# Performance work log

Measured on AMD Instinct MI355X. Metric: run time of the kernel, lower is better.

Reference implementation:

```python
import jax, jax.numpy as jnp
import numpy as np

N = 50000
E = 1600000
HID = 128
H = 8
D = HID // H


def _layer_norm(x, g, b, eps=1e-5):
    mu = jnp.mean(x, axis=-1, keepdims=True)
    var = jnp.mean(jnp.square(x - mu), axis=-1, keepdims=True)
    return (x - mu) * jax.lax.rsqrt(var + eps) * g + b


def setup_inputs() -> dict:
    key = jax.random.key(0)
    ks = jax.random.split(key, 20)
    s = 1.0 / np.sqrt(HID)
    inp = {
        "x": jax.random.normal(ks[0], (N, HID), jnp.float32),
        "edge_index": jax.random.randint(ks[1], (2, E), 0, N, jnp.int64),
        "edge_attr": jax.random.randint(ks[2], (E,), 0, 13, jnp.int64),
        # projections (stored as [in, out] so y = x @ W + b)
        "Wq": jax.random.normal(ks[3], (HID, HID), jnp.float32) * s,
        "bq": jnp.zeros((HID,), jnp.float32),
        "Wk": jax.random.normal(ks[4], (HID, HID), jnp.float32) * s,
        "bk": jnp.zeros((HID,), jnp.float32),
        "Wv": jax.random.normal(ks[5], (HID, HID), jnp.float32) * s,
        "bv": jnp.zeros((HID,), jnp.float32),
        "Wo": jax.random.normal(ks[6], (HID, HID), jnp.float32) * s,
        "bo": jnp.zeros((HID,), jnp.float32),
        "edge_bias_table": jax.random.normal(ks[7], (13, H), jnp.float32) * 0.02,
        "W1": jax.random.normal(ks[8], (HID, 4 * HID), jnp.float32) * s,
        "b1": jnp.zeros((4 * HID,), jnp.float32),
        "W2": jax.random.normal(ks[9], (4 * HID, HID), jnp.float32) * (0.5 * s),
        "b2": jnp.zeros((HID,), jnp.float32),
        "g1": jnp.ones((HID,), jnp.float32),
        "be1": jnp.zeros((HID,), jnp.float32),
        "g2": jnp.ones((HID,), jnp.float32),
        "be2": jnp.zeros((HID,), jnp.float32),
    }
    return inp


def reference(x, edge_index, edge_attr, Wq, bq, Wk, bk, Wv, bv, Wo, bo,
              edge_bias_table, W1, b1, W2, b2, g1, be1, g2, be2):
    n = x.shape[0]
    residual = x
    h = _layer_norm(x, g1, be1)
    Q = (h @ Wq + bq).reshape(n, H, D)
    K = (h @ Wk + bk).reshape(n, H, D)
    V = (h @ Wv + bv).reshape(n, H, D)
    src, dst = edge_index[0], edge_index[1]
    # per-edge scores [E, H]
    scores = jnp.sum(Q[dst] * K[src], axis=-1) / np.sqrt(D)
    scores = scores + edge_bias_table[jnp.clip(edge_attr, 0, 12)]
    # scatter softmax over incoming edges of each dst (global max, as in source)
    scores_exp = jnp.exp(scores - jnp.max(scores))
    attn_sum = jax.ops.segment_sum(scores_exp, dst, num_segments=n)  # [N, H]
    attn_w = scores_exp / (attn_sum[dst] + 1e-8)                      # [E, H]
    messages = V[src] * attn_w[..., None]                             # [E, H, D]
    out = jax.ops.segment_sum(messages, dst, num_segments=n)          # [N, H, D]
    out = out.reshape(n, HID) @ Wo + bo
    x = residual + out  # dropout is identity in eval
    residual = x
    h2 = _layer_norm(x, g2, be2)
    ffn = jax.nn.relu(h2 @ W1 + b1) @ W2 + b2
    return residual + ffn
```

## Files before the change

### kernel.cpp

```cpp
#include <hip/hip_runtime.h>
#include <hip/hip_bf16.h>

#define N_NODES 50000
#define E_EDGES 1600000
#define HID 128
#define NH 8
#define HD 16

#define NBKT 196
#define BKT_CAP 9216
#define CHUNK_A 4096
#define EPT 16
#define BINA_BLOCKS ((E_EDGES + CHUNK_A - 1) / CHUNK_A)
#define WCVT_BLOCKS 771
#define LN_BLOCKS 12500

using short8 = __attribute__((ext_vector_type(8))) short;
using f32x4  = __attribute__((ext_vector_type(4))) float;
using f32x2  = __attribute__((ext_vector_type(2))) float;
typedef _Float16 h16x2 __attribute__((ext_vector_type(2)));

#if defined(__has_builtin) && __has_builtin(__builtin_amdgcn_fdot2)
#define FDOT2(a, b, c) __builtin_amdgcn_fdot2((a), (b), (c), false)
#else
__device__ __forceinline__ float FDOT2(h16x2 a, h16x2 b, float c) {
    return fmaf((float)a[0], (float)b[0], fmaf((float)a[1], (float)b[1], c));
}
#endif

__device__ __forceinline__ float wave_reduce_sum(float v) {
    #pragma unroll
    for (int off = 32; off > 0; off >>= 1) v += __shfl_xor(v, off, 64);
    return v;
}

__device__ __forceinline__ unsigned int packbf2(float a, float b) {
    __hip_bfloat162 t;
    t.x = __float2bfloat16(a);
    t.y = __float2bfloat16(b);
    unsigned int u;
    __builtin_memcpy(&u, &t, 4);
    return u;
}

__device__ __forceinline__ unsigned char fp8e(float v) {
    return (unsigned char)(__builtin_amdgcn_cvt_pk_fp8_f32(v, v, 0u, false) & 0xFFu);
}

union U4H {
    uint4 u;
    h16x2 h[4];
};

struct KV {
    U4H k0, k1;
    uint4 v;
};

__global__ __launch_bounds__(256) void prep_kernel(
    const int* __restrict__ ei, const int* __restrict__ attr,
    int* __restrict__ bcur, unsigned int* __restrict__ temp,
    const float* __restrict__ Wq, const float* __restrict__ Wk,
    const float* __restrict__ Wv, const float* __restrict__ Wo,
    const float* __restrict__ W1, const float* __restrict__ W2,
    const float* __restrict__ bq, const float* __restrict__ bk,
    const float* __restrict__ bv,
    __hip_bfloat16* __restrict__ Wqkvt, __hip_bfloat16* __restrict__ Wot,
    __hip_bfloat16* __restrict__ W1t, __hip_bfloat16* __restrict__ W2t,
    float* __restrict__ bqkv,
    const float* __restrict__ x, const float* __restrict__ g1,
    const float* __restrict__ be1, __hip_bfloat16* __restrict__ h_out) {
    __shared__ unsigned int sval[CHUNK_A];
    __shared__ unsigned short sbkt[CHUNK_A];
    __shared__ int hist[NBKT];
    __shared__ int lofs[NBKT];
    __shared__ int gbase[NBKT];
    __shared__ int lcur[NBKT];
    __shared__ int sc[256];
    const int b = blockIdx.x;
    const int tid = threadIdx.x;
    if (b < BINA_BLOCKS) {
        const int e0 = b * CHUNK_A;
        const int n = min(CHUNK_A, E_EDGES - e0);
        for (int i = tid; i < NBKT; i += 256) hist[i] = 0;
        __syncthreads();
        unsigned int v[EPT];
        short bk_[EPT];
        #pragma unroll
        for (int j = 0; j < EPT; ++j) {
            int i = tid + j * 256;
            bk_[j] = -1;
            v[j] = 0;
            if (i < n) {
                int e = e0 + i;
                int src = ei[e];
                int dst = ei[E_EDGES + e];
                int a = attr[e]; a = min(max(a, 0), 12);
                v[j] = (unsigned)src | ((unsigned)a << 16) | ((unsigned)(dst & 255) << 20);
                int bb = dst >> 8;
                bk_[j] = (short)bb;
                atomicAdd(&hist[bb], 1);
            }
        }
        __syncthreads();
        sc[tid] = (tid < NBKT) ? hist[tid] : 0;
        __syncthreads();
        for (int off = 1; off < 256; off <<= 1) {
            int xx = (tid >= off) ? sc[tid - off] : 0;
            __syncthreads();
            sc[tid] += xx;
            __syncthreads();
        }
        if (tid < NBKT) {
            int h = hist[tid];
            lofs[tid] = sc[tid] - h;
            lcur[tid] = 0;
            gbase[tid] = h ? atomicAdd(&bcur[tid], h) : 0;
        }
        __syncthreads();
        #pragma unroll
        for (int j = 0; j < EPT; ++j) {
            if (bk_[j] >= 0) {
                int p = lofs[bk_[j]] + atomicAdd(&lcur[bk_[j]], 1);
                sval[p] = v[j];
                sbkt[p] = (unsigned short)bk_[j];
            }
        }
        __syncthreads();
        for (int i = tid; i < n; i += 256) {
            int bb = sbkt[i];
            temp[(size_t)bb * BKT_CAP + gbase[bb] + (i - lofs[bb])] = sval[i];
        }
    } else if (b < BINA_BLOCKS + WCVT_BLOCKS) {
        int t = (b - BINA_BLOCKS) * 256 + tid;
        if (t >= 196608) {
            int i = t - 196608;
            if (i < 384) bqkv[i] = i < 128 ? bq[i] : (i < 256 ? bk[i - 128] : bv[i - 256]);
            return;
        }
        const float* W; __hip_bfloat16* Wt; int K, N, idx;
        if (t < 65536) {
            int which = t >> 14; idx = t & 16383; K = 128; N = 128;
            W = which == 0 ? Wq : which == 1 ? Wk : which == 2 ? Wv : Wo;
            Wt = which == 3 ? Wot : Wqkvt + which * 16384;
        } else if (t < 131072) { idx = t - 65536;  K = 128; N = 512; W = W1; Wt = W1t; }
        else                   { idx = t - 131072; K = 512; N = 128; W = W2; Wt = W2t; }
        int n = idx / K, k = idx - n * K;
        Wt[idx] = __float2bfloat16(W[(size_t)k * N + n]);
    } else {
        int wave = tid >> 6;
        int lane = tid & 63;
        int row = (b - BINA_BLOCKS - WCVT_BLOCKS) * 4 + wave;
        if (row >= N_NODES) return;
        float2 v = ((const float2*)(x + (size_t)row * HID))[lane];
        float s = wave_reduce_sum(v.x + v.y);
        float mu = s * (1.0f / HID);
        float dx = v.x - mu, dy = v.y - mu;
        float q = wave_reduce_sum(dx * dx + dy * dy);
        float rstd = rsqrtf(q * (1.0f / HID) + 1e-5f);
        float2 gg = ((const float2*)g1)[lane];
        float2 bb = ((const float2*)be1)[lane];
        __hip_bfloat162 o;
        o.x = __float2bfloat16(dx * rstd * gg.x + bb.x);
        o.y = __float2bfloat16(dy * rstd * gg.y + bb.y);
        ((__hip_bfloat162*)(h_out + (size_t)row * HID))[lane] = o;
    }
}

template <int K, int OB>
__global__ __launch_bounds__(512) void gemm_mfma(const __hip_bfloat16* __restrict__ A,
                                                 const __hip_bfloat16* __restrict__ Wt,
                                                 const float* __restrict__ bias,
                                                 const float* __restrict__ res,
                                                 float* __restrict__ C,
                                                 __hip_bfloat16* __restrict__ Cb,
                                                 _Float16* __restrict__ Chh,
                                                 unsigned char* __restrict__ C8,
                                                 const float* __restrict__ gw,
                                                 const float* __restrict__ bw,
                                                 int M, int NC, int relu) {
    __shared__ short8 smem[2048 + 2048];
    const int row0 = blockIdx.x * 128;
    const int col0 = blockIdx.y * 128;
    const int tid = threadIdx.x;
    const int w = tid >> 6, l = tid & 63;
    const int lr = l & 15, hi = l >> 4;
    f32x4 acc[8] = {};
    for (int kk = 0; kk < K / 128; ++kk) {
        #pragma unroll
        for (int it = 0; it < 4; ++it) {
            unsigned d = tid + it * 512;
            int r = d >> 4, sd = d & 15;
            int ss = sd ^ (r & 7);
            int gr = row0 + r; if (gr >= M) gr = M - 1;
            __builtin_amdgcn_global_load_lds(
                (const __attribute__((address_space(1))) void*)(A + (size_t)gr * K + kk * 128 + ss * 8),
                (__attribute__((address_space(3))) void*)(smem + (d & ~63u)),
                16, 0, 0);
        }
        #pragma unroll
        for (int it = 0; it < 4; ++it) {
            unsigned d = tid + it * 512;
            int r = d >> 4, sd = d & 15;
            int ss = sd ^ (r & 7);
            __builtin_amdgcn_global_load_lds(
                (const __attribute__((address_space(1))) void*)(Wt + (size_t)(col0 + r) * K + kk * 128 + ss * 8),
                (__attribute__((address_space(3))) void*)(smem + 2048 + (d & ~63u)),
                16, 0, 0);
        }
        __syncthreads();
        const int ar = w * 16 + lr;
        #pragma unroll
        for (int ks = 0; ks < 4; ++ks) {
            int s = ks * 4 + hi;
            short8 a = smem[ar * 16 + (s ^ (ar & 7))];
            #pragma unroll
            for (int f = 0; f < 8; ++f) {
                int br = f * 16 + lr;
                short8 b = smem[2048 + br * 16 + (s ^ (br & 7))];
                acc[f] = __builtin_amdgcn_mfma_f32_16x16x32_bf16(a, b, acc[f], 0, 0, 0);
            }
        }
        __syncthreads();
    }
    if (OB == 3) {
        float vv[8][4];
        float gc[8], bc[8];
        #pragma unroll
        for (int f = 0; f < 8; ++f) {
            int c = f * 16 + lr;
            gc[f] = gw[c]; bc[f] = bw[c];
            float bv = bias[c];
            #pragma unroll
            for (int j = 0; j < 4; ++j) {
                int r = row0 + w * 16 + hi * 4 + j;
                int rr = r < M ? r : M - 1;
                vv[f][j] = acc[f][j] + bv + res[(size_t)rr * NC + c];
            }
        }
        #pragma unroll
        for (int j = 0; j < 4; ++j) {
            int r = row0 + w * 16 + hi * 4 + j;
            float s = 0.f, qq = 0.f;
            #pragma unroll
            for (int f = 0; f < 8; ++f) { s += vv[f][j]; qq += vv[f][j] * vv[f][j]; }
            #pragma unroll
            for (int m = 1; m <= 8; m <<= 1) { s += __shfl_xor(s, m); qq += __shfl_xor(qq, m); }
            float mu = s * (1.0f / 128.0f);
            float rstd = rsqrtf(qq * (1.0f / 128.0f) - mu * mu + 1e-5f);
            if (r < M) {
                #pragma unroll
                for (int f = 0; f < 8; ++f) {
                    int c = f * 16 + lr;
                    C[(size_t)r * NC + c] = vv[f][j];
                    Cb[(size_t)r * NC + c] = __float2bfloat16((vv[f][j] - mu) * rstd * gc[f] + bc[f]);
                }
            }
        }
        return;
    }
    const float scl = (OB == 2 && blockIdx.y == 0) ? 0.25f : 1.0f;
    #pragma unroll
    for (int f = 0; f < 8; ++f) {
        int c = col0 + f * 16 + lr;
        float bv = bias[c];
        #pragma unroll
        for (int j = 0; j < 4; ++j) {
            int r = row0 + w * 16 + hi * 4 + j;
            if (r < M) {
                float v = acc[f][j] + bv;
                if (relu) v = fmaxf(v, 0.f);
                if (res) v += res[(size_t)r * NC + c];
                if (OB == 0) C[(size_t)r * NC + c] = v;
                else if (OB == 1) Cb[(size_t)r * NC + c] = __float2bfloat16(v);
                else {
                    if (blockIdx.y < 2)
                        Chh[(size_t)blockIdx.y * N_NODES * 128 + (size_t)r * 128 + (c & 127)] =
                            (_Float16)(v * scl);
                    else
                        C8[(size_t)r * 128 + (c & 127)] = fp8e(v);
                }
            }
        }
    }
}

__global__ __launch_bounds__(1024) void binB_kernel(const int* __restrict__ bcur,
                                                    const unsigned int* __restrict__ temp,
                                                    unsigned int* __restrict__ packed,
                                                    int* __restrict__ offs) {
    __shared__ int cnts[256];
    __shared__ int hist[256];
    __shared__ int cur[256];
    const int b = blockIdx.x, tid = threadIdx.x;
    if (tid < 256) {
        cnts[tid] = (tid < NBKT) ? bcur[tid] : 0;
        hist[tid] = 0;
    }
    __syncthreads();
    for (int off = 1; off < 256; off <<= 1) {
        int x = 0;
        if (tid < 256 && tid >= off) x = cnts[tid - off];
        __syncthreads();
        if (tid < 256) cnts[tid] += x;
        __syncthreads();
    }
    const int cnt = bcur[b];
    const int start = cnts[b] - cnt;
    const size_t base = (size_t)b * BKT_CAP;
    for (int i = tid; i < cnt; i += 1024)
        atomicAdd(&hist[(temp[base + i] >> 20) & 255], 1);
    __syncthreads();
    if (tid < 256) cur[tid] = hist[tid];
    __syncthreads();
    for (int off = 1; off < 256; off <<= 1) {
        int x = 0;
        if (tid < 256 && tid >= off) x = cur[tid - off];
        __syncthreads();
        if (tid < 256) cur[tid] += x;
        __syncthreads();
    }
    const int node0 = b * 256;
    if (tid < 256) {
        int excl = cur[tid] - hist[tid];
        cur[tid] = excl;
        int node = node0 + tid;
        if (node < N_NODES) offs[node] = start + excl;
    }
    if (b == NBKT - 1 && tid == 0) offs[N_NODES] = start + cnt;
    __syncthreads();
    for (int i = tid; i < cnt; i += 1024) {
        unsigned int v = temp[base + i];
        int d = (v >> 20) & 255;
        int p = start + atomicAdd(&cur[d], 1);
        packed[p] = v & 0xFFFFFu;
    }
}

__global__ __launch_bounds__(256) void fused_attn_kernel(
    const unsigned int* __restrict__ packed,
    const int* __restrict__ offs,
    const _Float16* __restrict__ qkh,
    const unsigned char* __restrict__ v8p,
    const float* __restrict__ btab,
    __hip_bfloat16* __restrict__ out) {
    __shared__ float bLDS[104];
    const int tid = threadIdx.x;
    if (tid < 104) bLDS[tid] = btab[tid];
    __syncthreads();
    const int wave = tid >> 6, lane = tid & 63;
    const int n = blockIdx.x * 4 + wave;
    const int slot = lane >> 3, sub = lane & 7;
    const char* qh = (const char*)qkh;
    const char* kh = (const char*)(qkh + (size_t)N_NODES * 128);
    const unsigned sb = (unsigned)sub << 5;
    U4H q0, q1;
    q0.u = *(const uint4*)(qh + ((unsigned)n << 8) + sb);
    q1.u = *(const uint4*)(qh + ((unsigned)n << 8) + sb + 16u);
    const int lo = offs[n], hi = offs[n + 1];
    const int nit = (hi - lo + 7) >> 3;
    f32x2 acc2[8] = {};
    float wsum = 0.f;
    int i0 = lo + slot;
    bool vd0 = i0 < hi;           unsigned pk0 = vd0 ? packed[i0] : 0u;
    bool vd1 = i0 + 8 < hi;       unsigned pk1 = vd1 ? packed[i0 + 8] : 0u;
    bool vd2 = i0 + 16 < hi;      unsigned pk2 = vd2 ? packed[i0 + 16] : 0u;
    int inext = i0 + 24;
    KV kv0, kv1;
    {
        unsigned r0 = (pk0 & 0xFFFFu);
        kv0.k0.u = *(const uint4*)(kh + (r0 << 8) + sb);
        kv0.k1.u = *(const uint4*)(kh + (r0 << 8) + sb + 16u);
        kv0.v = *(const uint4*)(v8p + (r0 << 7) + (sb >> 1));
        unsigned r1 = (pk1 & 0xFFFFu);
        kv1.k0.u = *(const uint4*)(kh + (r1 << 8) + sb);
        kv1.k1.u = *(const uint4*)(kh + (r1 << 8) + sb + 16u);
        kv1.v = *(const uint4*)(v8p + (r1 << 7) + (sb >> 1));
    }
    for (int it = 0; it < nit; ++it) {
        const bool vd3 = inext < hi;
        const unsigned pk3 = vd3 ? packed[inext] : 0u;
        KV kv2;
        {
            unsigned r2 = (pk2 & 0xFFFFu);
            kv2.k0.u = *(const uint4*)(kh + (r2 << 8) + sb);
            kv2.k1.u = *(const uint4*)(kh + (r2 << 8) + sb + 16u);
            kv2.v = *(const uint4*)(v8p + (r2 << 7) + (sb >> 1));
        }
        float p = 0.f;
        #pragma unroll
        for (int j = 0; j < 4; ++j) p = FDOT2(q0.h[j], kv0.k0.h[j], p);
        #pragma unroll
        for (int j = 0; j < 4; ++j) p = FDOT2(q1.h[j], kv0.k1.h[j], p);
        float s = p + bLDS[((pk0 >> 16) & 0xFu) * 8 + sub];
        float w = vd0 ? __expf(s) : 0.f;
        wsum += w;
        f32x2 w2; w2[0] = w; w2[1] = w;
        f32x2 t;
        t = __builtin_amdgcn_cvt_pk_f32_fp8(kv0.v.x, false); acc2[0] = t * w2 + acc2[0];
        t = __builtin_amdgcn_cvt_pk_f32_fp8(kv0.v.x, true);  acc2[1] = t * w2 + acc2[1];
        t = __builtin_amdgcn_cvt_pk_f32_fp8(kv0.v.y, false); acc2[2] = t * w2 + acc2[2];
        t = __builtin_amdgcn_cvt_pk_f32_fp8(kv0.v.y, true);  acc2[3] = t * w2 + acc2[3];
        t = __builtin_amdgcn_cvt_pk_f32_fp8(kv0.v.z, false); acc2[4] = t * w2 + acc2[4];
        t = __builtin_amdgcn_cvt_pk_f32_fp8(kv0.v.z, true);  acc2[5] = t * w2 + acc2[5];
        t = __builtin_amdgcn_cvt_pk_f32_fp8(kv0.v.w, false); acc2[6] = t * w2 + acc2[6];
        t = __builtin_amdgcn_cvt_pk_f32_fp8(kv0.v.w, true);  acc2[7] = t * w2 + acc2[7];
        pk0 = pk1; vd0 = vd1;
        pk1 = pk2; vd1 = vd2;
        pk2 = pk3; vd2 = vd3;
        kv0 = kv1; kv1 = kv2;
        inext += 8;
    }
    float accf[16];
    #pragma unroll
    for (int j = 0; j < 8; ++j) { accf[2 * j] = acc2[j][0]; accf[2 * j + 1] = acc2[j][1]; }
    #pragma unroll
    for (int j = 0; j < 16; ++j) {
        accf[j] += __shfl_xor(accf[j], 8);
        accf[j] += __shfl_xor(accf[j], 16);
        accf[j] += __shfl_xor(accf[j], 32);
    }
    wsum += __shfl_xor(wsum, 8);
    wsum += __shfl_xor(wsum, 16);
    wsum += __shfl_xor(wsum, 32);
    if (slot == 0) {
        float inv = 1.0f / (wsum + 1e-8f);
        uint4 o0, o1;
        o0.x = packbf2(accf[0] * inv, accf[1] * inv);
        o0.y = packbf2(accf[2] * inv, accf[3] * inv);
        o0.z = packbf2(accf[4] * inv, accf[5] * inv);
        o0.w = packbf2(accf[6] * inv, accf[7] * inv);
        o1.x = packbf2(accf[8] * inv, accf[9] * inv);
        o1.y = packbf2(accf[10] * inv, accf[11] * inv);
        o1.z = packbf2(accf[12] * inv, accf[13] * inv);
        o1.w = packbf2(accf[14] * inv, accf[15] * inv);
        char* op = (char*)out + ((unsigned)n << 8) + ((unsigned)sub << 5);
        *(uint4*)op = o0;
        *(uint4*)(op + 16) = o1;
    }
}

extern "C" void kernel_launch(void* const* d_in, const int* in_sizes, int n_in,
                              void* d_out, int out_size, void* d_ws, size_t ws_size,
                              hipStream_t stream) {
    const float* x    = (const float*)d_in[0];
    const int*   ei   = (const int*)d_in[1];
    const int*   attr = (const int*)d_in[2];
    const float* Wq   = (const float*)d_in[3];
    const float* bq   = (const float*)d_in[4];
    const float* Wk   = (const float*)d_in[5];
    const float* bk   = (const float*)d_in[6];
    const float* Wv   = (const float*)d_in[7];
    const float* bv   = (const float*)d_in[8];
    const float* Wo   = (const float*)d_in[9];
    const float* bo   = (const float*)d_in[10];
    const float* ebt  = (const float*)d_in[11];
    const float* W1   = (const float*)d_in[12];
    const float* b1   = (const float*)d_in[13];
    const float* W2   = (const float*)d_in[14];
    const float* b2   = (const float*)d_in[15];
    const float* g1   = (const float*)d_in[16];
    const float* be1  = (const float*)d_in[17];
    const float* g2   = (const float*)d_in[18];
    const float* be2  = (const float*)d_in[19];
    float* out = (float*)d_out;

    char* ws = (char*)d_ws;
    const size_t szRowF = (size_t)N_NODES * HID * 4;
    const size_t szRowB = (size_t)N_NODES * HID * 2;
    const size_t ALIGN = 256;
    #define ALN(v) (((v) + ALIGN - 1) & ~(ALIGN - 1))
    size_t o = 0;
    __hip_bfloat16* h_buf = (__hip_bfloat16*)(ws + o); o += szRowB;
    _Float16* QKh = (_Float16*)(ws + o); o += (size_t)N_NODES * 256 * 2;
    unsigned char* V8 = (unsigned char*)(ws + o); o += (size_t)N_NODES * 128;
    unsigned int* packed = (unsigned int*)(ws + o); o += (size_t)E_EDGES * 4;
    unsigned int* temp = (unsigned int*)(ws + o); o += (size_t)NBKT * BKT_CAP * 4;
    int* bcur = (int*)(ws + o); o = ALN(o + (size_t)NBKT * 4);
    int* offs = (int*)(ws + o); o = ALN(o + (size_t)(N_NODES + 1) * 4);
    __hip_bfloat16* attn_ob = (__hip_bfloat16*)(ws + o); o += szRowB;
    float* x1 = (float*)(ws + o); o += szRowF;
    __hip_bfloat16* f1 = (__hip_bfloat16*)(ws + o); o += (size_t)N_NODES * 512 * 2;
    __hip_bfloat16* Wqkvt = (__hip_bfloat16*)(ws + o); o += 384 * 128 * 2;
    __hip_bfloat16* Wot = (__hip_bfloat16*)(ws + o); o += 128 * 128 * 2;
    __hip_bfloat16* W1t = (__hip_bfloat16*)(ws + o); o += 512 * 128 * 2;
    __hip_bfloat16* W2t = (__hip_bfloat16*)(ws + o); o += 128 * 512 * 2;
    float* bqkv = (float*)(ws + o); o += 384 * 4;
    __hip_bfloat16* h2 = h_buf;

    hipMemsetAsync(bcur, 0, (size_t)NBKT * 4, stream);

    prep_kernel<<<BINA_BLOCKS + WCVT_BLOCKS + LN_BLOCKS, 256, 0, stream>>>(
        ei, attr, bcur, temp,
        Wq, Wk, Wv, Wo, W1, W2, bq, bk, bv,
        Wqkvt, Wot, W1t, W2t, bqkv,
        x, g1, be1, h_buf);

    binB_kernel<<<NBKT, 1024, 0, stream>>>(bcur, temp, packed, offs);

    dim3 gqkv((N_NODES + 127) / 128, 3);
    gemm_mfma<128, 2><<<gqkv, 512, 0, stream>>>(h_buf, Wqkvt, bqkv, nullptr,
                                                nullptr, nullptr, QKh, V8,
                                                nullptr, nullptr, N_NODES, 384, 0);

    fused_attn_kernel<<<(N_NODES + 3) / 4, 256, 0, stream>>>(packed, offs, QKh, V8, ebt, attn_ob);

    dim3 gm((N_NODES + 127) / 128, 1);
    gemm_mfma<128, 3><<<gm, 512, 0, stream>>>(attn_ob, Wot, bo, x, x1,
                                              h2, nullptr, nullptr, g2, be2, N_NODES, 128, 0);

    dim3 gf1((N_NODES + 127) / 128, 4);
    gemm_mfma<128, 1><<<gf1, 512, 0, stream>>>(h2, W1t, b1, nullptr, nullptr,
                                               f1, nullptr, nullptr, nullptr, nullptr, N_NODES, 512, 1);
    gemm_mfma<512, 0><<<gm, 512, 0, stream>>>(f1, W2t, b2, x1, out,
                                              nullptr, nullptr, nullptr, nullptr, nullptr, N_NODES, 128, 0);
}
```

Before: 228.4 us.

## Merge edge bin-B pass with QKV GEMM and restructure attention gather pipeline

Folds the second binning pass (per-bucket histogram, scan and scatter into packed CSR) and the QKV projection GEMM into one launch. Block index picks between the binning role and the GEMM role, so the two independent stages can overlap on the GPU and one launch is removed. The binning blocks now run with 512 threads instead of 1024. The attention kernel's three-deep register pipeline of K/V gathers becomes a two-slot ping-pong that handles two edges per iteration through helper functions. This changes load prefetch depth and register pressure.

Result: faster. 220.6 us (-3.4%).

```diff
diff --git a/kernel.cpp b/kernel.cpp
--- a/kernel.cpp
+++ b/kernel.cpp
@@ -14,6 +14,7 @@
 #define BINA_BLOCKS ((E_EDGES + CHUNK_A - 1) / CHUNK_A)
 #define WCVT_BLOCKS 771
 #define LN_BLOCKS 12500
+#define QKV_XBLOCKS ((N_NODES + 127) / 128)
 
 using short8 = __attribute__((ext_vector_type(8))) short;
 using f32x4  = __attribute__((ext_vector_type(4))) float;
@@ -56,6 +57,39 @@
     U4H k0, k1;
     uint4 v;
 };
+
+__device__ __forceinline__ KV loadkv(const char* khs, const unsigned char* v8s, unsigned pk) {
+    KV r;
+    unsigned rr = pk & 0xFFFFu;
+    r.k0.u = *(const uint4*)(khs + (rr << 8));
+    r.k1.u = *(const uint4*)(khs + (rr << 8) + 16u);
+    r.v = *(const uint4*)(v8s + (rr << 7));
+    return r;
+}
+
+__device__ __forceinline__ void consume_kv(const KV& kv, unsigned pk, bool vd,
+                                           const U4H& q0, const U4H& q1,
+                                           const float* bLDS, int sub,
+                                           f32x2* acc2, float& wsum) {
+    float p = 0.f;
+    #pragma unroll
+    for (int j = 0; j < 4; ++j) p = FDOT2(q0.h[j], kv.k0.h[j], p);
+    #pragma unroll
+    for (int j = 0; j < 4; ++j) p = FDOT2(q1.h[j], kv.k1.h[j], p);
+    float s = p + bLDS[((pk >> 16) & 0xFu) * 8 + sub];
+    float w = vd ? __expf(s) : 0.f;
+    wsum += w;
+    f32x2 w2; w2[0] = w; w2[1] = w;
+    f32x2 t;
+    t = __builtin_amdgcn_cvt_pk_f32_fp8(kv.v.x, false); acc2[0] = t * w2 + acc2[0];
+    t = __builtin_amdgcn_cvt_pk_f32_fp8(kv.v.x, true);  acc2[1] = t * w2 + acc2[1];
+    t = __builtin_amdgcn_cvt_pk_f32_fp8(kv.v.y, false); acc2[2] = t * w2 + acc2[2];
+    t = __builtin_amdgcn_cvt_pk_f32_fp8(kv.v.y, true);  acc2[3] = t * w2 + acc2[3];
+    t = __builtin_amdgcn_cvt_pk_f32_fp8(kv.v.z, false); acc2[4] = t * w2 + acc2[4];
+    t = __builtin_amdgcn_cvt_pk_f32_fp8(kv.v.z, true);  acc2[5] = t * w2 + acc2[5];
+    t = __builtin_amdgcn_cvt_pk_f32_fp8(kv.v.w, false); acc2[6] = t * w2 + acc2[6];
+    t = __builtin_amdgcn_cvt_pk_f32_fp8(kv.v.w, true);  acc2[7] = t * w2 + acc2[7];
+}
 
 __global__ __launch_bounds__(256) void prep_kernel(
     const int* __restrict__ ei, const int* __restrict__ attr,
@@ -167,6 +201,125 @@
     }
 }
 
+__global__ __launch_bounds__(512) void qkv_binb_kernel(
+    const int* __restrict__ bcur, const unsigned int* __restrict__ temp,
+    unsigned int* __restrict__ packed, int* __restrict__ offs,
+    const __hip_bfloat16* __restrict__ A, const __hip_bfloat16* __restrict__ Wt,
+    const float* __restrict__ bias,
+    _Float16* __restrict__ Chh, unsigned char* __restrict__ C8, int M) {
+    __shared__ short8 smem[2048 + 2048];
+    const int tid = threadIdx.x;
+    if (blockIdx.x < NBKT) {
+        int* cnts = (int*)smem;
+        int* hist = cnts + 256;
+        int* cur = hist + 256;
+        const int b = blockIdx.x;
+        if (tid < 256) {
+            cnts[tid] = (tid < NBKT) ? bcur[tid] : 0;
+            hist[tid] = 0;
+        }
+        __syncthreads();
+        for (int off = 1; off < 256; off <<= 1) {
+            int x = 0;
+            if (tid < 256 && tid >= off) x = cnts[tid - off];
+            __syncthreads();
+            if (tid < 256) cnts[tid] += x;
+            __syncthreads();
+        }
+        const int cnt = bcur[b];
+        const int start = cnts[b] - cnt;
+        const size_t base = (size_t)b * BKT_CAP;
+        for (int i = tid; i < cnt; i += 512)
+            atomicAdd(&hist[(temp[base + i] >> 20) & 255], 1);
+        __syncthreads();
+        if (tid < 256) cur[tid] = hist[tid];
+        __syncthreads();
+        for (int off = 1; off < 256; off <<= 1) {
+            int x = 0;
+            if (tid < 256 && tid >= off) x = cur[tid - off];
+            __syncthreads();
+            if (tid < 256) cur[tid] += x;
+            __syncthreads();
+        }
+        const int node0 = b * 256;
+        if (tid < 256) {
+            int excl = cur[tid] - hist[tid];
+            cur[tid] = excl;
+            int node = node0 + tid;
+            if (node < N_NODES) offs[node] = start + excl;
+        }
+        if (b == NBKT - 1 && tid == 0) offs[N_NODES] = start + cnt;
+        __syncthreads();
+        for (int i = tid; i < cnt; i += 512) {
+            unsigned int v = temp[base + i];
+            int d = (v >> 20) & 255;
+            int p = start + atomicAdd(&cur[d], 1);
+            packed[p] = v & 0xFFFFFu;
+        }
+        return;
+    }
+    const int gb = blockIdx.x - NBKT;
+    const int plane = gb / QKV_XBLOCKS;
+    const int xb = gb - plane * QKV_XBLOCKS;
+    const int row0 = xb * 128;
+    const int col0 = plane * 128;
+    const int w = tid >> 6, l = tid & 63;
+    const int lr = l & 15, hi = l >> 4;
+    f32x4 acc[8] = {};
+    #pragma unroll
+    for (int it = 0; it < 4; ++it) {
+        unsigned d = tid + it * 512;
+        int r = d >> 4, sd = d & 15;
+        int ss = sd ^ (r & 7);
+        int gr = row0 + r; if (gr >= M) gr = M - 1;
+        __builtin_amdgcn_global_load_lds(
+            (const __attribute__((address_space(1))) void*)(A + (size_t)gr * 128 + ss * 8),
+            (__attribute__((address_space(3))) void*)(smem + (d & ~63u)),
+            16, 0, 0);
+    }
+    #pragma unroll
+    for (int it = 0; it < 4; ++it) {
+        unsigned d = tid + it * 512;
+        int r = d >> 4, sd = d & 15;
+        int ss = sd ^ (r & 7);
+        __builtin_amdgcn_global_load_lds(
+            (const __attribute__((address_space(1))) void*)(Wt + (size_t)(col0 + r) * 128 + ss * 8),
+            (__attribute__((address_space(3))) void*)(smem + 2048 + (d & ~63u)),
+            16, 0, 0);
+    }
+    __syncthreads();
+    const int ar = w * 16 + lr;
+    #pragma unroll
+    for (int ks = 0; ks < 4; ++ks) {
+        int s = ks * 4 + hi;
+        short8 a = smem[ar * 16 + (s ^ (ar & 7))];
+        #pragma unroll
+        for (int f = 0; f < 8; ++f) {
+            int br = f * 16 + lr;
+            short8 b = smem[2048 + br * 16 + (s ^ (br & 7))];
+            acc[f] = __builtin_amdgcn_mfma_f32_16x16x32_bf16(a, b, acc[f], 0, 0, 0);
+        }
+    }
+    const float scl = (plane == 0) ? 0.25f : 1.0f;
+    #pragma unroll
+    for (int f = 0; f < 8; ++f) {
+        int c = col0 + f * 16 + lr;
+        float bv = bias[c];
+        #pragma unroll
+        for (int j = 0; j < 4; ++j) {
+            int r = row0 + w * 16 + hi * 4 + j;
+            if (r < M) {
+                float v = acc[f][j] + bv;
+                if (plane < 2)
+                    Chh[(size_t)plane * N_NODES * 128 + (size_t)r * 128 + (c & 127)] =
+                        (_Float16)(v * scl);
+                else
+                    C8[(size_t)r * 128 + (c & 127)] = fp8e(v);
+            }
+        }
+    }
+}
+
 template <int K, int OB>
 __global__ __launch_bounds__(512) void gemm_mfma(const __hip_bfloat16* __restrict__ A,
                                                  const __hip_bfloat16* __restrict__ Wt,
@@ -174,8 +327,6 @@
                                                  const float* __restrict__ res,
                                                  float* __restrict__ C,
                                                  __hip_bfloat16* __restrict__ Cb,
-                                                 _Float16* __restrict__ Chh,
-                                                 unsigned char* __restrict__ C8,
                                                  const float* __restrict__ gw,
                                                  const float* __restrict__ bw,
                                                  int M, int NC, int relu) {
@@ -259,7 +410,6 @@
         }
         return;
     }
-    const float scl = (OB == 2 && blockIdx.y == 0) ? 0.25f : 1.0f;
     #pragma unroll
     for (int f = 0; f < 8; ++f) {
         int c = col0 + f * 16 + lr;
@@ -272,68 +422,9 @@
                 if (relu) v = fmaxf(v, 0.f);
                 if (res) v += res[(size_t)r * NC + c];
                 if (OB == 0) C[(size_t)r * NC + c] = v;
-                else if (OB == 1) Cb[(size_t)r * NC + c] = __float2bfloat16(v);
-                else {
-                    if (blockIdx.y < 2)
-                        Chh[(size_t)blockIdx.y * N_NODES * 128 + (size_t)r * 128 + (c & 127)] =
-                            (_Float16)(v * scl);
-                    else
-                        C8[(size_t)r * 128 + (c & 127)] = fp8e(v);
-                }
-            }
-        }
-    }
-}
-
-__global__ __launch_bounds__(1024) void binB_kernel(const int* __restrict__ bcur,
-                                                    const unsigned int* __restrict__ temp,
-                                                    unsigned int* __restrict__ packed,
-                                                    int* __restrict__ offs) {
-    __shared__ int cnts[256];
-    __shared__ int hist[256];
-    __shared__ int cur[256];
-    const int b = blockIdx.x, tid = threadIdx.x;
-    if (tid < 256) {
-        cnts[tid] = (tid < NBKT) ? bcur[tid] : 0;
-        hist[tid] = 0;
-    }
-    __syncthreads();
-    for (int off = 1; off < 256; off <<= 1) {
-        int x = 0;
-        if (tid < 256 && tid >= off) x = cnts[tid - off];
-        __syncthreads();
-        if (tid < 256) cnts[tid] += x;
-        __syncthreads();
-    }
-    const int cnt = bcur[b];
-    const int start = cnts[b] - cnt;
-    const size_t base = (size_t)b * BKT_CAP;
-    for (int i = tid; i < cnt; i += 1024)
-        atomicAdd(&hist[(temp[base + i] >> 20) & 255], 1);
-    __syncthreads();
-    if (tid < 256) cur[tid] = hist[tid];
-    __syncthreads();
-    for (int off = 1; off < 256; off <<= 1) {
-        int x = 0;
-        if (tid < 256 && tid >= off) x = cur[tid - off];
-        __syncthreads();
-        if (tid < 256) cur[tid] += x;
-        __syncthreads();
-    }
-    const int node0 = b * 256;
-    if (tid < 256) {
-        int excl = cur[tid] - hist[tid];
-        cur[tid] = excl;
-        int node = node0 + tid;
-        if (node < N_NODES) offs[node] = start + excl;
-    }
-    if (b == NBKT - 1 && tid == 0) offs[N_NODES] = start + cnt;
-    __syncthreads();
-    for (int i = tid; i < cnt; i += 1024) {
-        unsigned int v = temp[base + i];
-        int d = (v >> 20) & 255;
-        int p = start + atomicAdd(&cur[d], 1);
-        packed[p] = v & 0xFFFFFu;
+                else Cb[(size_t)r * NC + c] = __float2bfloat16(v);
+            }
+        }
     }
 }
 
@@ -352,8 +443,9 @@
     const int n = blockIdx.x * 4 + wave;
     const int slot = lane >> 3, sub = lane & 7;
     const char* qh = (const char*)qkh;
-    const char* kh = (const char*)(qkh + (size_t)N_NODES * 128);
     const unsigned sb = (unsigned)sub << 5;
+    const char* khs = (const char*)(qkh + (size_t)N_NODES * 128) + sb;
+    const unsigned char* v8s = v8p + (sb >> 1);
     U4H q0, q1;
     q0.u = *(const uint4*)(qh + ((unsigned)n << 8) + sb);
     q1.u = *(const uint4*)(qh + ((unsigned)n << 8) + sb + 16u);
@@ -361,56 +453,28 @@
     const int nit = (hi - lo + 7) >> 3;
     f32x2 acc2[8] = {};
     float wsum = 0.f;
-    int i0 = lo + slot;
-    bool vd0 = i0 < hi;           unsigned pk0 = vd0 ? packed[i0] : 0u;
-    bool vd1 = i0 + 8 < hi;       unsigned pk1 = vd1 ? packed[i0 + 8] : 0u;
-    bool vd2 = i0 + 16 < hi;      unsigned pk2 = vd2 ? packed[i0 + 16] : 0u;
-    int inext = i0 + 24;
-    KV kv0, kv1;
-    {
-        unsigned r0 = (pk0 & 0xFFFFu);
-        kv0.k0.u = *(const uint4*)(kh + (r0 << 8) + sb);
-        kv0.k1.u = *(const uint4*)(kh + (r0 << 8) + sb + 16u);
-        kv0.v = *(const uint4*)(v8p + (r0 << 7) + (sb >> 1));
-        unsigned r1 = (pk1 & 0xFFFFu);
-        kv1.k0.u = *(const uint4*)(kh + (r1 << 8) + sb);
-        kv1.k1.u = *(const uint4*)(kh + (r1 << 8) + sb + 16u);
-        kv1.v = *(const uint4*)(v8p + (r1 << 7) + (sb >> 1));
-    }
-    for (int it = 0; it < nit; ++it) {
-        const bool vd3 = inext < hi;
-        const unsigned pk3 = vd3 ? packed[inext] : 0u;
-        KV kv2;
-        {
-            unsigned r2 = (pk2 & 0xFFFFu);
-            kv2.k0.u = *(const uint4*)(kh + (r2 << 8) + sb);
-            kv2.k1.u = *(const uint4*)(kh + (r2 << 8) + sb + 16u);
-            kv2.v = *(const uint4*)(v8p + (r2 << 7) + (sb >> 1));
-        }
-        float p = 0.f;
-        #pragma unroll
-        for (int j = 0; j < 4; ++j) p = FDOT2(q0.h[j], kv0.k0.h[j], p);
-        #pragma unroll
-        for (int j = 0; j < 4; ++j) p = FDOT2(q1.h[j], kv0.k1.h[j], p);
-        float s = p + bLDS[((pk0 >> 16) & 0xFu) * 8 + sub];
-        float w = vd0 ? __expf(s) : 0.f;
-        wsum += w;
-        f32x2 w2; w2[0] = w; w2[1] = w;
-        f32x2 t;
-        t = __builtin_amdgcn_cvt_pk_f32_fp8(kv0.v.x, false); acc2[0] = t * w2 + acc2[0];
-        t = __builtin_amdgcn_cvt_pk_f32_fp8(kv0.v.x, true);  acc2[1] = t * w2 + acc2[1];
-        t = __builtin_amdgcn_cvt_pk_f32_fp8(kv0.v.y, false); acc2[2] = t * w2 + acc2[2];
-        t = __builtin_amdgcn_cvt_pk_f32_fp8(kv0.v.y, true);  acc2[3] = t * w2 + acc2[3];
-        t = __builtin_amdgcn_cvt_pk_f32_fp8(kv0.v.z, false); acc2[4] = t * w2 + acc2[4];
-        t = __builtin_amdgcn_cvt_pk_f32_fp8(kv0.v.z, true);  acc2[5] = t * w2 + acc2[5];
-        t = __builtin_amdgcn_cvt_pk_f32_fp8(kv0.v.w, false); acc2[6] = t * w2 + acc2[6];
-        t = __builtin_amdgcn_cvt_pk_f32_fp8(kv0.v.w, true);  acc2[7] = t * w2 + acc2[7];
-        pk0 = pk1; vd0 = vd1;
-        pk1 = pk2; vd1 = vd2;
-        pk2 = pk3; vd2 = vd3;
-        kv0 = kv1; kv1 = kv2;
-        inext += 8;
-    }
+    int i = lo + slot;
+    bool vd0 = i < hi;       unsigned pk0 = vd0 ? packed[i] : 0u;
+    bool vd1 = i + 8 < hi;   unsigned pk1 = vd1 ? packed[i + 8] : 0u;
+    KV a = loadkv(khs, v8s, pk0);
+    KV b = loadkv(khs, v8s, pk1);
+    int ii = i + 16;
+    int rem = nit;
+    while (rem >= 2) {
+        const bool vd2 = ii < hi;
+        const unsigned pk2 = vd2 ? packed[ii] : 0u;
+        const bool vd3 = ii + 8 < hi;
+        const unsigned pk3 = vd3 ? packed[ii + 8] : 0u;
+        consume_kv(a, pk0, vd0, q0, q1, bLDS, sub, acc2, wsum);
+        a = loadkv(khs, v8s, pk2);
+        consume_kv(b, pk1, vd1, q0, q1, bLDS, sub, acc2, wsum);
+        b = loadkv(khs, v8s, pk3);
+        pk0 = pk2; vd0 = vd2;
+        pk1 = pk3; vd1 = vd3;
+        ii += 16;
+        rem -= 2;
+    }
+    if (rem == 1) consume_kv(a, pk0, vd0, q0, q1, bLDS, sub, acc2, wsum);
     float accf[16];
     #pragma unroll
     for (int j = 0; j < 8; ++j) { accf[2 * j] = acc2[j][0]; accf[2 * j + 1] = acc2[j][1]; }
@@ -496,22 +560,19 @@
         Wqkvt, Wot, W1t, W2t, bqkv,
         x, g1, be1, h_buf);
 
-    binB_kernel<<<NBKT, 1024, 0, stream>>>(bcur, temp, packed, offs);
-
-    dim3 gqkv((N_NODES + 127) / 128, 3);
-    gemm_mfma<128, 2><<<gqkv, 512, 0, stream>>>(h_buf, Wqkvt, bqkv, nullptr,
-                                                nullptr, nullptr, QKh, V8,
-                                                nullptr, nullptr, N_NODES, 384, 0);
+    qkv_binb_kernel<<<NBKT + QKV_XBLOCKS * 3, 512, 0, stream>>>(
+        bcur, temp, packed, offs,
+        h_buf, Wqkvt, bqkv, QKh, V8, N_NODES);
 
     fused_attn_kernel<<<(N_NODES + 3) / 4, 256, 0, stream>>>(packed, offs, QKh, V8, ebt, attn_ob);
 
     dim3 gm((N_NODES + 127) / 128, 1);
     gemm_mfma<128, 3><<<gm, 512, 0, stream>>>(attn_ob, Wot, bo, x, x1,
-                                              h2, nullptr, nullptr, g2, be2, N_NODES, 128, 0);
+                                              h2, g2, be2, N_NODES, 128, 0);
 
     dim3 gf1((N_NODES + 127) / 128, 4);
     gemm_mfma<128, 1><<<gf1, 512, 0, stream>>>(h2, W1t, b1, nullptr, nullptr,
-                                               f1, nullptr, nullptr, nullptr, nullptr, N_NODES, 512, 1);
+                                               f1, nullptr, nullptr, N_NODES, 512, 1);
     gemm_mfma<512, 0><<<gm, 512, 0, stream>>>(f1, W2t, b2, x1, out,
-                                              nullptr, nullptr, nullptr, nullptr, nullptr, N_NODES, 128, 0);
-}
+                                              nullptr, nullptr, nullptr, N_NODES, 128, 0);
+}
```
